# Optimization experiments

Hardware: AMD Instinct MI355X
Metric: run time of the kernel (lower is better)

Reference implementation:

```python
import jax, jax.numpy as jnp
import numpy as np

SESSION_CHANNELS = [128, 160, 192, 224, 240, 248, 252, 256]  # per-session channel counts
N_SESS = len(SESSION_CHANNELS)
B, MAX_C, MAX_T = 16, 256, 4096
HID, N_SRC = 512, 256


def setup_inputs() -> dict:
    key = jax.random.key(0)
    ks = jax.random.split(key, 7)
    session_ids = jax.random.randint(ks[0], (B,), 0, N_SESS)
    chan_table = jnp.asarray(SESSION_CHANNELS)
    channel_counts = chan_table[session_ids]
    seq_lens = jax.random.randint(ks[1], (B,), MAX_T // 2, MAX_T + 1)
    x = jax.random.normal(ks[2], (B, MAX_C, MAX_T), jnp.float32)
    # zero-pad beyond true channels and true time (as the docstring states)
    cmask = (jnp.arange(MAX_C)[None, :] < channel_counts[:, None]).astype(x.dtype)
    tmask = (jnp.arange(MAX_T)[None, :] < seq_lens[:, None]).astype(x.dtype)
    x = x * cmask[:, :, None] * tmask[:, None, :]
    # per-session Linear(num_channels -> HID), padded to MAX_C rows (torch-style uniform init)
    lim1 = 1.0 / np.sqrt(MAX_C)
    W_sess = jax.random.uniform(ks[3], (N_SESS, MAX_C, HID), jnp.float32, -lim1, lim1)
    b_sess = jax.random.uniform(ks[4], (N_SESS, HID), jnp.float32, -lim1, lim1)
    lim2 = 1.0 / np.sqrt(HID)
    W2 = jax.random.uniform(ks[5], (HID, N_SRC), jnp.float32, -lim2, lim2)
    b2 = jax.random.uniform(ks[6], (N_SRC,), jnp.float32, -lim2, lim2)
    return dict(x=x, session_ids=session_ids, channel_counts=channel_counts,
                seq_lens=seq_lens, W_sess=W_sess, b_sess=b_sess, W2=W2, b2=b2)


def reference(x, session_ids, channel_counts, seq_lens, W_sess, b_sess, W2, b2):
    # mask padded channels so the full-width contraction equals the sliced per-sample matmul
    cmask = (jnp.arange(x.shape[1])[None, :] < channel_counts[:, None]).astype(x.dtype)
    xm = x * cmask[:, :, None]                       # (B, Max_C, Max_T)
    W = W_sess[session_ids]                          # (B, Max_C, HID) gathered per sample
    b = b_sess[session_ids]                          # (B, HID)
    h = jnp.einsum('bct,bch->bht', xm, W) + b[:, :, None]
    h = jax.nn.gelu(h, approximate=False)            # torch nn.GELU default is exact erf
    out = jnp.einsum('bht,hs->bst', h, W2) + b2[None, :, None]  # (B, N_SRC, Max_T)
    tmask = (jnp.arange(x.shape[2])[None, :] < seq_lens[:, None]).astype(x.dtype)
    return out * tmask[:, None, :]
```

## Files before the change

kernel.cpp:

```cpp
#include <hip/hip_runtime.h>

typedef __attribute__((ext_vector_type(8))) _Float16 f16x8;
typedef __attribute__((ext_vector_type(4))) _Float16 f16x4;
typedef __attribute__((ext_vector_type(2))) __fp16 fp16v2;
typedef __attribute__((ext_vector_type(4))) float f32x4;

#define NB 16
#define MAXC 256
#define MAXT 4096
#define HID 512
#define NSRC 256

#define BARV() asm volatile("s_waitcnt vmcnt(0) lgkmcnt(0)\n\ts_barrier" ::: "memory")
#define BAR() asm volatile("s_waitcnt lgkmcnt(0)\n\ts_barrier" ::: "memory")

#define MFMA(a, b, c) __builtin_amdgcn_mfma_f32_16x16x32_f16(a, b, c, 0, 0, 0)

typedef __attribute__((address_space(1))) const void gconst_void;
typedef __attribute__((address_space(3))) void lds_void;
#define GLOAD16(gp, lp) \
  __builtin_amdgcn_global_load_lds((gconst_void*)(gp), (lds_void*)(lp), 16, 0, 0)

__device__ __forceinline__ float gelu_fast(float x) {
  float p = x * x;
  float q = __builtin_fmaf(p, -0.10294336f, -2.30220778f);
  float e = __builtin_amdgcn_exp2f(x * q);
  return x * __builtin_amdgcn_rcpf(1.0f + e);
}

__global__ void transpose_cvt_kernel(const float* __restrict__ src,
                                     _Float16* __restrict__ dst, int R, int C) {
  __shared__ float tile[32][33];
  const float* s = src + (size_t)blockIdx.z * R * C;
  _Float16* d = dst + (size_t)blockIdx.z * R * C;
  int c0 = blockIdx.x * 32, r0 = blockIdx.y * 32;
  int tx = threadIdx.x, ty = threadIdx.y;
  for (int i = ty; i < 32; i += 8)
    tile[i][tx] = s[(size_t)(r0 + i) * C + (c0 + tx)];
  __syncthreads();
  for (int i = ty; i < 32; i += 8)
    d[(size_t)(c0 + i) * R + (r0 + tx)] = (_Float16)tile[tx][i];
}

__global__ __launch_bounds__(256)
void transpose_x_kernel(const float* __restrict__ x,
                        const int* __restrict__ seq_lens,
                        const int* __restrict__ chan_counts,
                        _Float16* __restrict__ xT) {
  int b = blockIdx.z;
  int seqlen = seq_lens[b];
  int t0 = blockIdx.x * 64;
  if (t0 >= ((seqlen + 127) & ~127)) return;
  int c0 = blockIdx.y * 64;
  int tid = threadIdx.x;
  int wt = tid >> 5;
  int c2 = (tid & 31) * 2;
  _Float16* op = xT + ((size_t)b * MAXT + t0) * MAXC + c0;

  if (c0 >= chan_counts[b]) {
    #pragma unroll
    for (int i = 0; i < 8; ++i) {
      fp16v2 z = {(_Float16)0.f, (_Float16)0.f};
      *(fp16v2*)(op + (size_t)(wt + i * 8) * MAXC + c2) = z;
    }
    return;
  }

  __shared__ float tile[64][65];
  int tx = tid & 63, ty = tid >> 6;
  const float* xp = x + ((size_t)b * MAXC + c0) * MAXT + t0;
  #pragma unroll
  for (int i = 0; i < 16; ++i) {
    int c = ty + i * 4;
    tile[c][tx] = xp[(size_t)c * MAXT + tx];
  }
  __syncthreads();
  #pragma unroll
  for (int i = 0; i < 8; ++i) {
    int tl = wt + i * 8;
    fp16v2 p = __builtin_amdgcn_cvt_pkrtz(tile[c2][tl], tile[c2 + 1][tl]);
    *(fp16v2*)(op + (size_t)tl * MAXC + c2) = p;
  }
}


__global__ __launch_bounds__(256, 4)
void gemm1_kernel(const _Float16* __restrict__ xT,
                  const int* __restrict__ sess_ids,
                  const int* __restrict__ seq_lens,
                  const _Float16* __restrict__ W1t,
                  const float* __restrict__ b_sess,
                  _Float16* __restrict__ h_t) {
  int wg = blockIdx.x;
  int nt = wg & 31;
  int mt = (wg >> 5) & 3;
  int b = wg >> 7;
  int tb0 = nt * 128, h0 = mt * 128;
  int seqlen = seq_lens[b];
  if (tb0 >= seqlen) return;
  int sid = sess_ids[b];

  __shared__ _Float16 As[128 * 64];
  __shared__ _Float16 Bs[128 * 64];

  int tid = threadIdx.x;
  int lane = tid & 63, w = tid >> 6;
  int wr = w >> 1, wc = w & 1;
  int lg = lane >> 4, lr = lane & 15;

  f32x4 acc[4][4];
  #pragma unroll
  for (int mi = 0; mi < 4; ++mi) {
    f32x4 bv = *(const f32x4*)(b_sess + sid * HID + h0 + wr * 64 + mi * 16 + lg * 4);
    #pragma unroll
    for (int ni = 0; ni < 4; ++ni) acc[mi][ni] = bv;
  }

  int rsub = lane >> 3;
  int swb = ((lane & 7) ^ rsub) * 16;
  const char* gA = (const char*)(W1t + (size_t)sid * HID * MAXC + (size_t)h0 * MAXC)
                   + (size_t)(w * 32 + rsub) * 512 + swb;
  const char* gB = (const char*)(xT + ((size_t)b * MAXT + tb0) * MAXC)
                   + (size_t)(w * 32 + rsub) * 512 + swb;
  char* lA = (char*)As + w * 4096;
  char* lB = (char*)Bs + w * 4096;

#define STAGE1(kc)                                                   \
  _Pragma("unroll")                                                  \
  for (int j = 0; j < 4; ++j) {                                      \
    GLOAD16(gA + (size_t)(kc)*128 + (size_t)j * 8 * 512, lA + j * 1024); \
    GLOAD16(gB + (size_t)(kc)*128 + (size_t)j * 8 * 512, lB + j * 1024); \
  }

  STAGE1(0);
  BARV();

  #pragma unroll 1
  for (int kc = 0; kc < 4; ++kc) {
    #pragma unroll
    for (int slot = 0; slot < 2; ++slot) {
      f16x8 af[4], bf[4];
      #pragma unroll
      for (int mi = 0; mi < 4; ++mi) {
        int row = wr * 64 + mi * 16 + lr;
        af[mi] = *(const f16x8*)(&As[row * 64 + (((slot * 4 + lg) ^ (row & 7)) * 8)]);
      }
      #pragma unroll
      for (int ni = 0; ni < 4; ++ni) {
        int t = wc * 64 + ni * 16 + lr;
        bf[ni] = *(const f16x8*)(&Bs[t * 64 + (((slot * 4 + lg) ^ (t & 7)) * 8)]);
      }
      __builtin_amdgcn_s_setprio(1);
      #pragma unroll
      for (int mi = 0; mi < 4; ++mi)
        #pragma unroll
        for (int ni = 0; ni < 4; ++ni)
          acc[mi][ni] = MFMA(af[mi], bf[ni], acc[mi][ni]);
      __builtin_amdgcn_s_setprio(0);
    }
    if (kc < 3) {
      BAR();
      STAGE1(kc + 1);
      BARV();
    }
  }

  _Float16* hp = h_t + (size_t)b * MAXT * HID;
  #pragma unroll
  for (int mi = 0; mi < 4; ++mi) {
    int h = h0 + wr * 64 + mi * 16 + lg * 4;
    #pragma unroll
    for (int ni = 0; ni < 4; ++ni) {
      int t = tb0 + wc * 64 + ni * 16 + lr;
      f16x4 g;
      #pragma unroll
      for (int r = 0; r < 4; ++r) g[r] = (_Float16)gelu_fast(acc[mi][ni][r]);
      *(f16x4*)(hp + (size_t)t * HID + h) = g;
    }
  }
}

__global__ __launch_bounds__(256, 4)
void gemm2_kernel(const int* __restrict__ seq_lens,
                  const _Float16* __restrict__ W2t,
                  const float* __restrict__ b2,
                  const _Float16* __restrict__ h_t,
                  float* __restrict__ out) {
  int wg = blockIdx.x;
  int nt = wg & 31;
  int mt = (wg >> 5) & 1;
  int b = wg >> 6;
  int tb0 = nt * 128, s0 = mt * 128;
  int seqlen = seq_lens[b];
  int tid = threadIdx.x;

  if (tb0 >= seqlen) {
    int sr = tid >> 1, tq = (tid & 1) * 64;
    float* po = out + ((size_t)b * NSRC + s0 + sr) * MAXT + tb0 + tq;
    f32x4 z = {0.f, 0.f, 0.f, 0.f};
    #pragma unroll
    for (int i = 0; i < 16; ++i) *(f32x4*)(po + i * 4) = z;
    return;
  }

  __shared__ _Float16 As[128 * 64];
  __shared__ _Float16 Bs[128 * 64];

  int lane = tid & 63, w = tid >> 6;
  int wr = w >> 1, wc = w & 1;
  int lg = lane >> 4, lr = lane & 15;

  f32x4 acc[4][4];
  #pragma unroll
  for (int mi = 0; mi < 4; ++mi) {
    f32x4 bv = *(const f32x4*)(b2 + s0 + wr * 64 + mi * 16 + lg * 4);
    #pragma unroll
    for (int ni = 0; ni < 4; ++ni) acc[mi][ni] = bv;
  }

  int rsub = lane >> 3;
  int swb = ((lane & 7) ^ rsub) * 16;
  const char* gA = (const char*)(W2t + (size_t)s0 * HID)
                   + (size_t)(w * 32 + rsub) * 1024 + swb;
  const char* gB = (const char*)(h_t + ((size_t)b * MAXT + tb0) * HID)
                   + (size_t)(w * 32 + rsub) * 1024 + swb;
  char* lA = (char*)As + w * 4096;
  char* lB = (char*)Bs + w * 4096;

#define STAGE2(kc)                                                    \
  _Pragma("unroll")                                                   \
  for (int j = 0; j < 4; ++j) {                                       \
    GLOAD16(gA + (size_t)(kc)*128 + (size_t)j * 8 * 1024, lA + j * 1024); \
    GLOAD16(gB + (size_t)(kc)*128 + (size_t)j * 8 * 1024, lB + j * 1024); \
  }

  STAGE2(0);
  BARV();

  #pragma unroll 1
  for (int kc = 0; kc < 8; ++kc) {
    #pragma unroll
    for (int slot = 0; slot < 2; ++slot) {
      f16x8 af[4], bf[4];
      #pragma unroll
      for (int mi = 0; mi < 4; ++mi) {
        int row = wr * 64 + mi * 16 + lr;
        af[mi] = *(const f16x8*)(&As[row * 64 + (((slot * 4 + lg) ^ (row & 7)) * 8)]);
      }
      #pragma unroll
      for (int ni = 0; ni < 4; ++ni) {
        int t = wc * 64 + ni * 16 + lr;
        bf[ni] = *(const f16x8*)(&Bs[t * 64 + (((slot * 4 + lg) ^ (t & 7)) * 8)]);
      }
      __builtin_amdgcn_s_setprio(1);
      #pragma unroll
      for (int mi = 0; mi < 4; ++mi)
        #pragma unroll
        for (int ni = 0; ni < 4; ++ni)
          acc[mi][ni] = MFMA(af[mi], bf[ni], acc[mi][ni]);
      __builtin_amdgcn_s_setprio(0);
    }
    if (kc < 7) {
      BAR();
      STAGE2(kc + 1);
      BARV();
    }
  }

  #pragma unroll
  for (int mi = 0; mi < 4; ++mi) {
    int s = s0 + wr * 64 + mi * 16 + lg * 4;
    #pragma unroll
    for (int ni = 0; ni < 4; ++ni) {
      int t = tb0 + wc * 64 + ni * 16 + lr;
      float m = (t < seqlen) ? 1.0f : 0.0f;
      #pragma unroll
      for (int r = 0; r < 4; ++r)
        out[((size_t)b * NSRC + s + r) * MAXT + t] = acc[mi][ni][r] * m;
    }
  }
}

extern "C" void kernel_launch(void* const* d_in, const int* in_sizes, int n_in,
                              void* d_out, int out_size, void* d_ws, size_t ws_size,
                              hipStream_t stream) {
  const float* x      = (const float*)d_in[0];
  const int* sess     = (const int*)d_in[1];
  const int* ccnt     = (const int*)d_in[2];
  const int* seq      = (const int*)d_in[3];
  const float* W_sess = (const float*)d_in[4];
  const float* b_sess = (const float*)d_in[5];
  const float* W2     = (const float*)d_in[6];
  const float* b2     = (const float*)d_in[7];
  float* out = (float*)d_out;

  char* wp = (char*)d_ws;
  _Float16* W1t = (_Float16*)wp;                     wp += (size_t)8 * HID * MAXC * 2;
  _Float16* W2t = (_Float16*)wp;                     wp += (size_t)NSRC * HID * 2;
  _Float16* h_t = (_Float16*)wp;                     wp += (size_t)NB * MAXT * HID * 2;
  _Float16* xT  = (_Float16*)wp;

  dim3 tb(32, 8);
  transpose_cvt_kernel<<<dim3(HID / 32, MAXC / 32, 8), tb, 0, stream>>>(W_sess, W1t, MAXC, HID);
  transpose_cvt_kernel<<<dim3(NSRC / 32, HID / 32, 1), tb, 0, stream>>>(W2, W2t, HID, NSRC);
  transpose_x_kernel<<<dim3(MAXT / 64, MAXC / 64, NB), dim3(256), 0, stream>>>(x, seq, ccnt, xT);

  gemm1_kernel<<<dim3(NB * 4 * 32), dim3(256), 0, stream>>>(xT, sess, seq, W1t, b_sess, h_t);
  gemm2_kernel<<<dim3(NB * 2 * 32), dim3(256), 0, stream>>>(seq, W2t, b2, h_t, out);
}
```

Measured before the change: 82.13 us.

## Keep full-K x tile resident in LDS and loop over all hidden blocks in gemm1

gemm1 now assigns each workgroup a 64-timestep tile and loads its full 256-channel x slice into LDS once. It then iterates over all four 128-wide hidden blocks, streaming only W1 chunks and writing each GELU output block as it finishes. This removes the fourfold redundant reads of x across hidden tiles. The cost is fewer workgroups (1024 instead of 2048), half the MFMA tile per wave, a longer serial loop with a barrier every step, and more LDS, with launch bounds lowered to 3.

```diff
diff --git a/kernel.cpp b/kernel.cpp
--- a/kernel.cpp
+++ b/kernel.cpp
@@ -84,7 +84,7 @@
 }
 
 
-__global__ __launch_bounds__(256, 4)
+__global__ __launch_bounds__(256, 3)
 void gemm1_kernel(const _Float16* __restrict__ xT,
                   const int* __restrict__ sess_ids,
                   const int* __restrict__ seq_lens,
@@ -92,91 +92,115 @@
                   const float* __restrict__ b_sess,
                   _Float16* __restrict__ h_t) {
   int wg = blockIdx.x;
-  int nt = wg & 31;
-  int mt = (wg >> 5) & 3;
-  int b = wg >> 7;
-  int tb0 = nt * 128, h0 = mt * 128;
+  int nt = wg & 63;
+  int b = wg >> 6;
+  int t0 = nt * 64;
   int seqlen = seq_lens[b];
-  if (tb0 >= seqlen) return;
+  if (t0 >= seqlen) return;
   int sid = sess_ids[b];
 
+  __shared__ _Float16 Bs[64 * 256];
   __shared__ _Float16 As[128 * 64];
-  __shared__ _Float16 Bs[128 * 64];
 
   int tid = threadIdx.x;
   int lane = tid & 63, w = tid >> 6;
   int wr = w >> 1, wc = w & 1;
   int lg = lane >> 4, lr = lane & 15;
 
-  f32x4 acc[4][4];
-  #pragma unroll
-  for (int mi = 0; mi < 4; ++mi) {
-    f32x4 bv = *(const f32x4*)(b_sess + sid * HID + h0 + wr * 64 + mi * 16 + lg * 4);
-    #pragma unroll
-    for (int ni = 0; ni < 4; ++ni) acc[mi][ni] = bv;
+  {
+    int l5 = lane >> 5, sl = lane & 31;
+    const char* gB = (const char*)(xT + ((size_t)b * MAXT + t0) * MAXC);
+    char* lB = (char*)Bs;
+    #pragma unroll
+    for (int j = 0; j < 8; ++j) {
+      int g = w * 8 + j;
+      int t = g * 2 + l5;
+      int gc = (sl & 24) | ((sl & 7) ^ (t & 7));
+      GLOAD16(gB + (size_t)t * 512 + gc * 16, lB + g * 1024);
+    }
   }
 
   int rsub = lane >> 3;
   int swb = ((lane & 7) ^ rsub) * 16;
-  const char* gA = (const char*)(W1t + (size_t)sid * HID * MAXC + (size_t)h0 * MAXC)
-                   + (size_t)(w * 32 + rsub) * 512 + swb;
-  const char* gB = (const char*)(xT + ((size_t)b * MAXT + tb0) * MAXC)
+  const char* gA = (const char*)(W1t + (size_t)sid * HID * MAXC)
                    + (size_t)(w * 32 + rsub) * 512 + swb;
   char* lA = (char*)As + w * 4096;
-  char* lB = (char*)Bs + w * 4096;
-
-#define STAGE1(kc)                                                   \
-  _Pragma("unroll")                                                  \
-  for (int j = 0; j < 4; ++j) {                                      \
-    GLOAD16(gA + (size_t)(kc)*128 + (size_t)j * 8 * 512, lA + j * 1024); \
-    GLOAD16(gB + (size_t)(kc)*128 + (size_t)j * 8 * 512, lB + j * 1024); \
-  }
-
-  STAGE1(0);
+
+#define STAGE_A(p)                                                            \
+  {                                                                           \
+    int nh0 = (p) >> 2, nkc = (p) & 3;                                        \
+    _Pragma("unroll")                                                         \
+    for (int j = 0; j < 4; ++j)                                               \
+      GLOAD16(gA + (size_t)nh0 * 65536 + nkc * 128 + (size_t)j * 4096,        \
+              lA + j * 1024);                                                 \
+  }
+
+  STAGE_A(0);
+
+  f32x4 acc[4][2];
+  #pragma unroll
+  for (int mi = 0; mi < 4; ++mi) {
+    f32x4 bv = *(const f32x4*)(b_sess + sid * HID + wr * 64 + mi * 16 + lg * 4);
+    #pragma unroll
+    for (int ni = 0; ni < 2; ++ni) acc[mi][ni] = bv;
+  }
+
   BARV();
 
+  _Float16* hp = h_t + (size_t)b * MAXT * HID;
+
   #pragma unroll 1
-  for (int kc = 0; kc < 4; ++kc) {
+  for (int p = 0; p < 16; ++p) {
+    int kc = p & 3;
     #pragma unroll
     for (int slot = 0; slot < 2; ++slot) {
-      f16x8 af[4], bf[4];
+      f16x8 af[4], bf[2];
       #pragma unroll
       for (int mi = 0; mi < 4; ++mi) {
         int row = wr * 64 + mi * 16 + lr;
         af[mi] = *(const f16x8*)(&As[row * 64 + (((slot * 4 + lg) ^ (row & 7)) * 8)]);
       }
       #pragma unroll
-      for (int ni = 0; ni < 4; ++ni) {
-        int t = wc * 64 + ni * 16 + lr;
-        bf[ni] = *(const f16x8*)(&Bs[t * 64 + (((slot * 4 + lg) ^ (t & 7)) * 8)]);
+      for (int ni = 0; ni < 2; ++ni) {
+        int t = wc * 32 + ni * 16 + lr;
+        bf[ni] = *(const f16x8*)(&Bs[t * 256 + kc * 64 + (((slot * 4 + lg) ^ (t & 7)) * 8)]);
       }
       __builtin_amdgcn_s_setprio(1);
       #pragma unroll
       for (int mi = 0; mi < 4; ++mi)
         #pragma unroll
-        for (int ni = 0; ni < 4; ++ni)
+        for (int ni = 0; ni < 2; ++ni)
           acc[mi][ni] = MFMA(af[mi], bf[ni], acc[mi][ni]);
       __builtin_amdgcn_s_setprio(0);
     }
-    if (kc < 3) {
+    if (p < 15) {
       BAR();
-      STAGE1(kc + 1);
-      BARV();
-    }
-  }
-
-  _Float16* hp = h_t + (size_t)b * MAXT * HID;
-  #pragma unroll
-  for (int mi = 0; mi < 4; ++mi) {
-    int h = h0 + wr * 64 + mi * 16 + lg * 4;
-    #pragma unroll
-    for (int ni = 0; ni < 4; ++ni) {
-      int t = tb0 + wc * 64 + ni * 16 + lr;
-      f16x4 g;
-      #pragma unroll
-      for (int r = 0; r < 4; ++r) g[r] = (_Float16)gelu_fast(acc[mi][ni][r]);
-      *(f16x4*)(hp + (size_t)t * HID + h) = g;
-    }
+      STAGE_A(p + 1);
+    }
+    if (kc == 3) {
+      int h0 = p >> 2;
+      #pragma unroll
+      for (int mi = 0; mi < 4; ++mi) {
+        int h = h0 * 128 + wr * 64 + mi * 16 + lg * 4;
+        #pragma unroll
+        for (int ni = 0; ni < 2; ++ni) {
+          int t = t0 + wc * 32 + ni * 16 + lr;
+          f16x4 g;
+          #pragma unroll
+          for (int r = 0; r < 4; ++r) g[r] = (_Float16)gelu_fast(acc[mi][ni][r]);
+          *(f16x4*)(hp + (size_t)t * HID + h) = g;
+        }
+      }
+      if (p < 15) {
+        #pragma unroll
+        for (int mi = 0; mi < 4; ++mi) {
+          f32x4 bv = *(const f32x4*)(b_sess + sid * HID + (h0 + 1) * 128 + wr * 64 + mi * 16 + lg * 4);
+          #pragma unroll
+          for (int ni = 0; ni < 2; ++ni) acc[mi][ni] = bv;
+        }
+      }
+    }
+    if (p < 15) BARV();
   }
 }
 
@@ -305,6 +329,6 @@
   transpose_cvt_kernel<<<dim3(NSRC / 32, HID / 32, 1), tb, 0, stream>>>(W2, W2t, HID, NSRC);
   transpose_x_kernel<<<dim3(MAXT / 64, MAXC / 64, NB), dim3(256), 0, stream>>>(x, seq, ccnt, xT);
 
-  gemm1_kernel<<<dim3(NB * 4 * 32), dim3(256), 0, stream>>>(xT, sess, seq, W1t, b_sess, h_t);
+  gemm1_kernel<<<dim3(NB * 64), dim3(256), 0, stream>>>(xT, sess, seq, W1t, b_sess, h_t);
   gemm2_kernel<<<dim3(NB * 2 * 32), dim3(256), 0, stream>>>(seq, W2t, b2, h_t, out);
 }
```

Measured after the change: 93.83 us. 14.2% more time.

## Double-buffer LDS tiles in both GEMMs with partial vmcnt waits

Applied to the files above, without the earlier changes.

Both GEMM kernels now keep two LDS buffers for the A and B tiles and prefetch the k-chunk two steps ahead. A partial s_waitcnt vmcnt(8) lets the next chunk's loads stay in flight while the current chunk is consumed, so global-to-LDS latency overlaps with MFMA work. LDS use per block doubles, so the launch-bounds occupancy hint drops from 4 to 2 blocks per CU, which reduces latency hiding across waves.

```diff
diff --git a/kernel.cpp b/kernel.cpp
--- a/kernel.cpp
+++ b/kernel.cpp
@@ -11,8 +11,9 @@
 #define HID 512
 #define NSRC 256
 
-#define BARV() asm volatile("s_waitcnt vmcnt(0) lgkmcnt(0)\n\ts_barrier" ::: "memory")
-#define BAR() asm volatile("s_waitcnt lgkmcnt(0)\n\ts_barrier" ::: "memory")
+#define WARBAR() asm volatile("s_waitcnt lgkmcnt(0)\n\ts_barrier" ::: "memory")
+#define RDYBAR8() asm volatile("s_waitcnt vmcnt(8)\n\ts_barrier" ::: "memory")
+#define RDYBAR0() asm volatile("s_waitcnt vmcnt(0) lgkmcnt(0)\n\ts_barrier" ::: "memory")
 
 #define MFMA(a, b, c) __builtin_amdgcn_mfma_f32_16x16x32_f16(a, b, c, 0, 0, 0)
 
@@ -84,7 +85,7 @@
 }
 
 
-__global__ __launch_bounds__(256, 4)
+__global__ __launch_bounds__(256, 2)
 void gemm1_kernel(const _Float16* __restrict__ xT,
                   const int* __restrict__ sess_ids,
                   const int* __restrict__ seq_lens,
@@ -100,8 +101,8 @@
   if (tb0 >= seqlen) return;
   int sid = sess_ids[b];
 
-  __shared__ _Float16 As[128 * 64];
-  __shared__ _Float16 Bs[128 * 64];
+  __shared__ _Float16 As[2][128 * 64];
+  __shared__ _Float16 Bs[2][128 * 64];
 
   int tid = threadIdx.x;
   int lane = tid & 63, w = tid >> 6;
@@ -122,33 +123,35 @@
                    + (size_t)(w * 32 + rsub) * 512 + swb;
   const char* gB = (const char*)(xT + ((size_t)b * MAXT + tb0) * MAXC)
                    + (size_t)(w * 32 + rsub) * 512 + swb;
-  char* lA = (char*)As + w * 4096;
-  char* lB = (char*)Bs + w * 4096;
-
-#define STAGE1(kc)                                                   \
-  _Pragma("unroll")                                                  \
-  for (int j = 0; j < 4; ++j) {                                      \
-    GLOAD16(gA + (size_t)(kc)*128 + (size_t)j * 8 * 512, lA + j * 1024); \
-    GLOAD16(gB + (size_t)(kc)*128 + (size_t)j * 8 * 512, lB + j * 1024); \
-  }
-
-  STAGE1(0);
-  BARV();
+
+#define STAGE1(kc, bb)                                                        \
+  _Pragma("unroll")                                                           \
+  for (int j = 0; j < 4; ++j) {                                               \
+    GLOAD16(gA + (size_t)(kc)*128 + (size_t)j * 8 * 512,                      \
+            (char*)As[bb] + w * 4096 + j * 1024);                             \
+    GLOAD16(gB + (size_t)(kc)*128 + (size_t)j * 8 * 512,                      \
+            (char*)Bs[bb] + w * 4096 + j * 1024);                             \
+  }
+
+  STAGE1(0, 0);
+  STAGE1(1, 1);
+  RDYBAR8();
 
   #pragma unroll 1
   for (int kc = 0; kc < 4; ++kc) {
+    int cur = kc & 1;
     #pragma unroll
     for (int slot = 0; slot < 2; ++slot) {
       f16x8 af[4], bf[4];
       #pragma unroll
       for (int mi = 0; mi < 4; ++mi) {
         int row = wr * 64 + mi * 16 + lr;
-        af[mi] = *(const f16x8*)(&As[row * 64 + (((slot * 4 + lg) ^ (row & 7)) * 8)]);
+        af[mi] = *(const f16x8*)(&As[cur][row * 64 + (((slot * 4 + lg) ^ (row & 7)) * 8)]);
       }
       #pragma unroll
       for (int ni = 0; ni < 4; ++ni) {
         int t = wc * 64 + ni * 16 + lr;
-        bf[ni] = *(const f16x8*)(&Bs[t * 64 + (((slot * 4 + lg) ^ (t & 7)) * 8)]);
+        bf[ni] = *(const f16x8*)(&Bs[cur][t * 64 + (((slot * 4 + lg) ^ (t & 7)) * 8)]);
       }
       __builtin_amdgcn_s_setprio(1);
       #pragma unroll
@@ -158,10 +161,12 @@
           acc[mi][ni] = MFMA(af[mi], bf[ni], acc[mi][ni]);
       __builtin_amdgcn_s_setprio(0);
     }
-    if (kc < 3) {
-      BAR();
-      STAGE1(kc + 1);
-      BARV();
+    if (kc < 2) {
+      WARBAR();
+      STAGE1(kc + 2, cur);
+      RDYBAR8();
+    } else if (kc == 2) {
+      RDYBAR0();
     }
   }
 
@@ -180,7 +185,7 @@
   }
 }
 
-__global__ __launch_bounds__(256, 4)
+__global__ __launch_bounds__(256, 2)
 void gemm2_kernel(const int* __restrict__ seq_lens,
                   const _Float16* __restrict__ W2t,
                   const float* __restrict__ b2,
@@ -203,8 +208,8 @@
     return;
   }
 
-  __shared__ _Float16 As[128 * 64];
-  __shared__ _Float16 Bs[128 * 64];
+  __shared__ _Float16 As[2][128 * 64];
+  __shared__ _Float16 Bs[2][128 * 64];
 
   int lane = tid & 63, w = tid >> 6;
   int wr = w >> 1, wc = w & 1;
@@ -224,33 +229,35 @@
                    + (size_t)(w * 32 + rsub) * 1024 + swb;
   const char* gB = (const char*)(h_t + ((size_t)b * MAXT + tb0) * HID)
                    + (size_t)(w * 32 + rsub) * 1024 + swb;
-  char* lA = (char*)As + w * 4096;
-  char* lB = (char*)Bs + w * 4096;
-
-#define STAGE2(kc)                                                    \
-  _Pragma("unroll")                                                   \
-  for (int j = 0; j < 4; ++j) {                                       \
-    GLOAD16(gA + (size_t)(kc)*128 + (size_t)j * 8 * 1024, lA + j * 1024); \
-    GLOAD16(gB + (size_t)(kc)*128 + (size_t)j * 8 * 1024, lB + j * 1024); \
-  }
-
-  STAGE2(0);
-  BARV();
+
+#define STAGE2(kc, bb)                                                        \
+  _Pragma("unroll")                                                           \
+  for (int j = 0; j < 4; ++j) {                                               \
+    GLOAD16(gA + (size_t)(kc)*128 + (size_t)j * 8 * 1024,                     \
+            (char*)As[bb] + w * 4096 + j * 1024);                             \
+    GLOAD16(gB + (size_t)(kc)*128 + (size_t)j * 8 * 1024,                     \
+            (char*)Bs[bb] + w * 4096 + j * 1024);                             \
+  }
+
+  STAGE2(0, 0);
+  STAGE2(1, 1);
+  RDYBAR8();
 
   #pragma unroll 1
   for (int kc = 0; kc < 8; ++kc) {
+    int cur = kc & 1;
     #pragma unroll
     for (int slot = 0; slot < 2; ++slot) {
       f16x8 af[4], bf[4];
       #pragma unroll
       for (int mi = 0; mi < 4; ++mi) {
         int row = wr * 64 + mi * 16 + lr;
-        af[mi] = *(const f16x8*)(&As[row * 64 + (((slot * 4 + lg) ^ (row & 7)) * 8)]);
+        af[mi] = *(const f16x8*)(&As[cur][row * 64 + (((slot * 4 + lg) ^ (row & 7)) * 8)]);
       }
       #pragma unroll
       for (int ni = 0; ni < 4; ++ni) {
         int t = wc * 64 + ni * 16 + lr;
-        bf[ni] = *(const f16x8*)(&Bs[t * 64 + (((slot * 4 + lg) ^ (t & 7)) * 8)]);
+        bf[ni] = *(const f16x8*)(&Bs[cur][t * 64 + (((slot * 4 + lg) ^ (t & 7)) * 8)]);
       }
       __builtin_amdgcn_s_setprio(1);
       #pragma unroll
@@ -260,10 +267,12 @@
           acc[mi][ni] = MFMA(af[mi], bf[ni], acc[mi][ni]);
       __builtin_amdgcn_s_setprio(0);
     }
-    if (kc < 7) {
-      BAR();
-      STAGE2(kc + 1);
-      BARV();
+    if (kc < 6) {
+      WARBAR();
+      STAGE2(kc + 2, cur);
+      RDYBAR8();
+    } else if (kc == 6) {
+      RDYBAR0();
     }
   }
 
```

New measurement: 86.29 us. 1.05x slower.

## Merge prep transposes into one kernel and enlarge gemm1 tile to 256 rows

Applied to the files above, without the earlier changes.

Three preprocessing launches (two weight transposes and the x transpose) become a single prep kernel that picks its role from the block index, removing launch overhead and gaps between launches. gemm1 moves to 512-thread blocks covering 256 hidden rows per tile, so each xT tile is loaded once per half of HID instead of once per quarter, and more A rows share each B load. The risk is that the compute part of gemm1 (not shown) may still index with the old wave layout. Occupancy also changes under the new launch bounds.

```diff
diff --git a/kernel.cpp b/kernel.cpp
--- a/kernel.cpp
+++ b/kernel.cpp
@@ -28,31 +28,50 @@
   return x * __builtin_amdgcn_rcpf(1.0f + e);
 }
 
-__global__ void transpose_cvt_kernel(const float* __restrict__ src,
-                                     _Float16* __restrict__ dst, int R, int C) {
+__device__ __forceinline__ void transpose_cvt_tile(const float* src, _Float16* dst,
+                                                   int R, int C, int cx, int ry,
+                                                   int tid) {
   __shared__ float tile[32][33];
-  const float* s = src + (size_t)blockIdx.z * R * C;
-  _Float16* d = dst + (size_t)blockIdx.z * R * C;
-  int c0 = blockIdx.x * 32, r0 = blockIdx.y * 32;
-  int tx = threadIdx.x, ty = threadIdx.y;
+  int c0 = cx * 32, r0 = ry * 32;
+  int tx = tid & 31, ty = tid >> 5;
   for (int i = ty; i < 32; i += 8)
-    tile[i][tx] = s[(size_t)(r0 + i) * C + (c0 + tx)];
+    tile[i][tx] = src[(size_t)(r0 + i) * C + (c0 + tx)];
   __syncthreads();
   for (int i = ty; i < 32; i += 8)
-    d[(size_t)(c0 + i) * R + (r0 + tx)] = (_Float16)tile[tx][i];
+    dst[(size_t)(c0 + i) * R + (r0 + tx)] = (_Float16)tile[tx][i];
 }
 
 __global__ __launch_bounds__(256)
-void transpose_x_kernel(const float* __restrict__ x,
-                        const int* __restrict__ seq_lens,
-                        const int* __restrict__ chan_counts,
-                        _Float16* __restrict__ xT) {
-  int b = blockIdx.z;
+void prep_kernel(const float* __restrict__ x,
+                 const int* __restrict__ seq_lens,
+                 const int* __restrict__ chan_counts,
+                 const float* __restrict__ W_sess,
+                 const float* __restrict__ W2,
+                 _Float16* __restrict__ xT,
+                 _Float16* __restrict__ W1t,
+                 _Float16* __restrict__ W2t) {
+  int wg = blockIdx.x;
+  int tid = threadIdx.x;
+
+  if (wg >= 4096) {
+    if (wg >= 5120) {
+      int idx = wg - 5120;
+      transpose_cvt_tile(W2, W2t, HID, NSRC, idx & 7, idx >> 3, tid);
+    } else {
+      int idx = wg - 4096;
+      int z = idx >> 7;
+      transpose_cvt_tile(W_sess + (size_t)z * MAXC * HID,
+                         W1t + (size_t)z * MAXC * HID,
+                         MAXC, HID, idx & 15, (idx >> 4) & 7, tid);
+    }
+    return;
+  }
+
+  int b = wg >> 8;
+  int t0 = (wg & 63) * 64;
+  int c0 = ((wg >> 6) & 3) * 64;
   int seqlen = seq_lens[b];
-  int t0 = blockIdx.x * 64;
   if (t0 >= ((seqlen + 127) & ~127)) return;
-  int c0 = blockIdx.y * 64;
-  int tid = threadIdx.x;
   int wt = tid >> 5;
   int c2 = (tid & 31) * 2;
   _Float16* op = xT + ((size_t)b * MAXT + t0) * MAXC + c0;
@@ -84,7 +103,7 @@
 }
 
 
-__global__ __launch_bounds__(256, 4)
+__global__ __launch_bounds__(512, 2)
 void gemm1_kernel(const _Float16* __restrict__ xT,
                   const int* __restrict__ sess_ids,
                   const int* __restrict__ seq_lens,
@@ -93,14 +112,14 @@
                   _Float16* __restrict__ h_t) {
   int wg = blockIdx.x;
   int nt = wg & 31;
-  int mt = (wg >> 5) & 3;
-  int b = wg >> 7;
-  int tb0 = nt * 128, h0 = mt * 128;
+  int mt = (wg >> 5) & 1;
+  int b = wg >> 6;
+  int tb0 = nt * 128, h0 = mt * 256;
   int seqlen = seq_lens[b];
   if (tb0 >= seqlen) return;
   int sid = sess_ids[b];
 
-  __shared__ _Float16 As[128 * 64];
+  __shared__ _Float16 As[256 * 64];
   __shared__ _Float16 Bs[128 * 64];
 
   int tid = threadIdx.x;
@@ -121,15 +140,18 @@
   const char* gA = (const char*)(W1t + (size_t)sid * HID * MAXC + (size_t)h0 * MAXC)
                    + (size_t)(w * 32 + rsub) * 512 + swb;
   const char* gB = (const char*)(xT + ((size_t)b * MAXT + tb0) * MAXC)
-                   + (size_t)(w * 32 + rsub) * 512 + swb;
+                   + (size_t)(w * 16 + rsub) * 512 + swb;
   char* lA = (char*)As + w * 4096;
-  char* lB = (char*)Bs + w * 4096;
-
-#define STAGE1(kc)                                                   \
-  _Pragma("unroll")                                                  \
-  for (int j = 0; j < 4; ++j) {                                      \
-    GLOAD16(gA + (size_t)(kc)*128 + (size_t)j * 8 * 512, lA + j * 1024); \
-    GLOAD16(gB + (size_t)(kc)*128 + (size_t)j * 8 * 512, lB + j * 1024); \
+  char* lB = (char*)Bs + w * 2048;
+
+#define STAGE1(kc)                                                        \
+  {                                                                       \
+    _Pragma("unroll")                                                     \
+    for (int j = 0; j < 4; ++j)                                           \
+      GLOAD16(gA + (size_t)(kc)*128 + (size_t)j * 8 * 512, lA + j * 1024); \
+    _Pragma("unroll")                                                     \
+    for (int j = 0; j < 2; ++j)                                           \
+      GLOAD16(gB + (size_t)(kc)*128 + (size_t)j * 8 * 512, lB + j * 1024); \
   }
 
   STAGE1(0);
@@ -300,11 +322,8 @@
   _Float16* h_t = (_Float16*)wp;                     wp += (size_t)NB * MAXT * HID * 2;
   _Float16* xT  = (_Float16*)wp;
 
-  dim3 tb(32, 8);
-  transpose_cvt_kernel<<<dim3(HID / 32, MAXC / 32, 8), tb, 0, stream>>>(W_sess, W1t, MAXC, HID);
-  transpose_cvt_kernel<<<dim3(NSRC / 32, HID / 32, 1), tb, 0, stream>>>(W2, W2t, HID, NSRC);
-  transpose_x_kernel<<<dim3(MAXT / 64, MAXC / 64, NB), dim3(256), 0, stream>>>(x, seq, ccnt, xT);
-
-  gemm1_kernel<<<dim3(NB * 4 * 32), dim3(256), 0, stream>>>(xT, sess, seq, W1t, b_sess, h_t);
+  prep_kernel<<<dim3(4096 + 1024 + 128), dim3(256), 0, stream>>>(
+      x, seq, ccnt, W_sess, W2, xT, W1t, W2t);
+  gemm1_kernel<<<dim3(NB * 2 * 32), dim3(512), 0, stream>>>(xT, sess, seq, W1t, b_sess, h_t);
   gemm2_kernel<<<dim3(NB * 2 * 32), dim3(256), 0, stream>>>(seq, W2t, b2, h_t, out);
 }
```

New measurement: 76.88 us. 6.4% less time.
